# Performance work log

Measured on AMD Instinct MI355X. Metric: run time of the kernel, lower is better.

The kernel has to match this reference:

```python
import jax, jax.numpy as jnp
import numpy as np

DEPTH = 8
IN_FEATURES = 512
OUT_FEATURES = 256
LEAF_COUNT = 2 ** DEPTH          # 256
GATE_COUNT = LEAF_COUNT - 1      # 255
BATCH = 65536


def setup_inputs() -> dict:
    key = jax.random.key(0)
    k1, k2, k3 = jax.random.split(key, 3)
    x = jax.random.normal(k1, (BATCH, IN_FEATURES), dtype=jnp.float32)
    # gw stored transposed as (in_features, gate_count), kaiming-like scale
    gw = jax.random.normal(k2, (IN_FEATURES, GATE_COUNT), dtype=jnp.float32) * (1.0 / np.sqrt(IN_FEATURES))
    gb = jnp.zeros((GATE_COUNT,), dtype=jnp.float32)
    z = jax.random.normal(k3, (OUT_FEATURES, LEAF_COUNT), dtype=jnp.float32)
    return {"x": x, "gw": gw, "gb": gb, "z": z}


def _leaf_probs(x, gw, gb):
    # gatings: (B, gate_count); node it's left child (2p+1) uses g, right child (2p+2) uses 1-g
    g = jax.nn.sigmoid(x @ gw + gb)
    B = x.shape[0]
    dens = jnp.ones((B, 1), dtype=x.dtype)
    for d in range(DEPTH):  # level-wise vectorized traversal, O(depth) steps
        lo, hi = 2 ** d - 1, 2 ** (d + 1) - 1
        gl = g[:, lo:hi]  # (B, 2^d) gatings at this level
        # interleave [parent*g, parent*(1-g)] -> children order matches heap layout
        dens = jnp.stack([dens * gl, dens * (1.0 - gl)], axis=-1).reshape(B, -1)
    return dens  # (B, leaf_count)


def reference(x, gw, gb, z):
    leaf = _leaf_probs(x, gw, gb)        # (B, L)
    # constant projection: z @ leaf_probs^T, then transpose -> (B, out)
    return leaf @ z.T
```

## Files before the change

kernel.cpp:

```cpp
#include <hip/hip_runtime.h>
#include <hip/hip_bf16.h>
#include <stdint.h>


typedef short bf16x8 __attribute__((ext_vector_type(8)));
typedef float f32x4  __attribute__((ext_vector_type(4)));

__device__ __forceinline__ unsigned short f2bf(float f) {
    union { float f; uint32_t u; } c; c.f = f;
    uint32_t u = c.u;
    return (unsigned short)((u + 0x7FFFu + ((u >> 16) & 1u)) >> 16);
}

__device__ __forceinline__ uint32_t pkbf(float a, float b) {
    union { __hip_bfloat162 h; uint32_t u; } cv;
    cv.h = __float22bfloat162_rn(make_float2(a, b));
    return cv.u;
}

__global__ __launch_bounds__(256) void softtree_prep(
    const float* __restrict__ gw, const float* __restrict__ z,
    unsigned short* __restrict__ gwt, unsigned short* __restrict__ zb)
{
    if (blockIdx.x < 32) {
        __shared__ float tsm[64][65];
        const int k0 = (blockIdx.x >> 2) * 64;
        const int n0 = (blockIdx.x & 3) * 64;
        const int r = threadIdx.x >> 6;
        const int c = threadIdx.x & 63;
        const int n = n0 + c;
        #pragma unroll
        for (int i = 0; i < 16; ++i) {
            int kk = r + i * 4;
            tsm[kk][c] = (n < 255) ? gw[(size_t)(k0 + kk) * 255 + n] : 0.0f;
        }
        __syncthreads();
        #pragma unroll
        for (int i = 0; i < 16; ++i) {
            int nn = r + i * 4;
            gwt[(size_t)(n0 + nn) * 512 + k0 + c] = f2bf(tsm[c][nn]);
        }
    } else {
        int base = (blockIdx.x - 32) * 1024 + threadIdx.x * 4;
        const float4 v = *(const float4*)(z + base);
        ushort4 o;
        o.x = f2bf(v.x); o.y = f2bf(v.y); o.z = f2bf(v.z); o.w = f2bf(v.w);
        *(ushort4*)(zb + base) = o;
    }
}

__global__ __launch_bounds__(512, 4) void softtree_main(
    const float* __restrict__ x, const float* __restrict__ gb,
    const unsigned short* __restrict__ gwt, const unsigned short* __restrict__ zb,
    float* __restrict__ out)
{
    __shared__ char smraw[81920];
    float* gs = (float*)smraw;

    const int tid  = threadIdx.x;
    const int lane = tid & 63;
    const int wv   = tid >> 6;
    const int q    = lane >> 4;
    const int l15  = lane & 15;
    const int wr   = wv & 3;
    const int wc   = wv >> 2;
    const int R0   = blockIdx.x * 128;

    const int xrow = tid >> 3;
    const int xkg  = (tid & 7) ^ (xrow & 7);
    const float* xp0 = x + (size_t)(R0 + xrow) * 512 + xkg * 8;
    const float* xp1 = xp0 + (size_t)64 * 512;
    char* xsw0 = smraw + 65536 + tid * 16;
    char* xsw1 = xsw0 + 8192;

    const int ggate_b = wv * 32 + (lane >> 3);
    const int gkg     = (lane & 7) ^ ((lane >> 3) & 7);
    const unsigned short* gwp[4];
    #pragma unroll
    for (int j = 0; j < 4; ++j)
        gwp[j] = gwt + (size_t)(ggate_b + j * 8) * 512 + gkg * 8;
    const uint32_t gwLds = (uint32_t)(wv * 4) * 1024;

    f32x4 acc[2][8];
    #pragma unroll
    for (int t = 0; t < 2; ++t)
        #pragma unroll
        for (int i = 0; i < 8; ++i) acc[t][i] = (f32x4){0.f, 0.f, 0.f, 0.f};

    float4 xa0 = *(const float4*)(xp0);
    float4 xb0 = *(const float4*)(xp0 + 4);
    float4 xa1 = *(const float4*)(xp1);
    float4 xb1 = *(const float4*)(xp1 + 4);
    #pragma unroll
    for (int j = 0; j < 4; ++j)
        __builtin_amdgcn_global_load_lds(
            (const __attribute__((address_space(1))) void*)(gwp[j]),
            (__attribute__((address_space(3))) void*)(smraw + gwLds + j * 1024),
            16, 0, 0);

    for (int kc = 0; kc < 8; ++kc) {
        const int buf = kc & 1;
        __syncthreads();

        union { uint4 u4; uint32_t u[4]; } w0, w1;
        w0.u[0] = pkbf(xa0.x, xa0.y); w0.u[1] = pkbf(xa0.z, xa0.w);
        w0.u[2] = pkbf(xb0.x, xb0.y); w0.u[3] = pkbf(xb0.z, xb0.w);
        w1.u[0] = pkbf(xa1.x, xa1.y); w1.u[1] = pkbf(xa1.z, xa1.w);
        w1.u[2] = pkbf(xb1.x, xb1.y); w1.u[3] = pkbf(xb1.z, xb1.w);
        *(uint4*)xsw0 = w0.u4;
        *(uint4*)xsw1 = w1.u4;

        __syncthreads();

        if (kc < 7) {
            const int ko = (kc + 1) * 64;
            #pragma unroll
            for (int j = 0; j < 4; ++j)
                __builtin_amdgcn_global_load_lds(
                    (const __attribute__((address_space(1))) void*)(gwp[j] + ko),
                    (__attribute__((address_space(3))) void*)(smraw + (buf ^ 1) * 32768 + gwLds + j * 1024),
                    16, 0, 0);
            xa0 = *(const float4*)(xp0 + ko);
            xb0 = *(const float4*)(xp0 + ko + 4);
            xa1 = *(const float4*)(xp1 + ko);
            xb1 = *(const float4*)(xp1 + ko + 4);
        }

        #pragma unroll
        for (int s = 0; s < 2; ++s) {
            const int jx = (4 * s + q) ^ (l15 & 7);
            bf16x8 a0 = *(const bf16x8*)(smraw + 65536 + ((16 * wr + l15) * 8 + jx) * 16);
            bf16x8 a1 = *(const bf16x8*)(smraw + 65536 + 8192 + ((16 * wr + l15) * 8 + jx) * 16);
            #pragma unroll
            for (int nt = 0; nt < 8; ++nt) {
                const int gate = 128 * wc + nt * 16 + l15;
                bf16x8 b = *(const bf16x8*)(smraw + buf * 32768 + (gate * 8 + jx) * 16);
                acc[0][nt] = __builtin_amdgcn_mfma_f32_16x16x32_bf16(a0, b, acc[0][nt], 0, 0, 0);
                acc[1][nt] = __builtin_amdgcn_mfma_f32_16x16x32_bf16(a1, b, acc[1][nt], 0, 0, 0);
            }
        }
    }

    float gbv[8];
    #pragma unroll
    for (int nt = 0; nt < 8; ++nt) {
        int col = 128 * wc + nt * 16 + l15;
        gbv[nt] = (col < 255) ? gb[col] : 0.0f;
    }

    for (int t = 0; t < 2; ++t) {
        __syncthreads();

        #pragma unroll
        for (int nt = 0; nt < 8; ++nt) {
            const int col = 128 * wc + nt * 16 + l15;
            #pragma unroll
            for (int r = 0; r < 4; ++r) {
                const int rowl = 16 * wr + 4 * q + r;
                float v = acc[t][nt][r] + gbv[nt];
                gs[rowl * 258 + col] = 1.0f / (1.0f + __expf(-v));
            }
        }
        __syncthreads();

        const float* gr = gs + (16 * wr + l15) * 258;
        float g0v = gr[0];
        float t1v[2] = { g0v, 1.0f - g0v };
        float t2v[4], t3v[8];
        #pragma unroll
        for (int u = 0; u < 2; ++u) {
            float gl = gr[1 + u];
            t2v[2 * u] = t1v[u] * gl; t2v[2 * u + 1] = t1v[u] - t2v[2 * u];
        }
        #pragma unroll
        for (int u = 0; u < 4; ++u) {
            float gl = gr[3 + u];
            t3v[2 * u] = t2v[u] * gl; t3v[2 * u + 1] = t2v[u] - t3v[2 * u];
        }
        bf16x8 a2[8];
        #pragma unroll
        for (int c = 0; c < 8; ++c) {
            const int G = c * 4 + q;
            float p = t3v[c];
            float g3 = gr[7 + c];
            p = (q & 2) ? (p - p * g3) : (p * g3);
            float g4 = gr[15 + 2 * c + (q >> 1)];
            p = (q & 1) ? (p - p * g4) : (p * g4);
            float g5 = gr[31 + G];
            float a0 = p * g5, a1 = p - a0;
            float g6a = gr[63 + 2 * G], g6b = gr[64 + 2 * G];
            float b00 = a0 * g6a, b01 = a0 - b00;
            float b10 = a1 * g6b, b11 = a1 - b10;
            float g70 = gr[127 + 4 * G], g71 = gr[128 + 4 * G];
            float g72 = gr[129 + 4 * G], g73 = gr[130 + 4 * G];
            float lf0 = b00 * g70, lf1 = b00 - lf0;
            float lf2 = b01 * g71, lf3 = b01 - lf2;
            float lf4 = b10 * g72, lf5 = b10 - lf4;
            float lf6 = b11 * g73, lf7 = b11 - lf6;
            union { bf16x8 v; uint32_t u[4]; } pk;
            pk.u[0] = pkbf(lf0, lf1);
            pk.u[1] = pkbf(lf2, lf3);
            pk.u[2] = pkbf(lf4, lf5);
            pk.u[3] = pkbf(lf6, lf7);
            a2[c] = pk.v;
        }

        f32x4 acc2[8];
        #pragma unroll
        for (int i = 0; i < 8; ++i) acc2[i] = (f32x4){0.f, 0.f, 0.f, 0.f};
        #pragma unroll
        for (int nt = 0; nt < 8; ++nt) {
            const unsigned short* zrow = zb + (size_t)(128 * wc + nt * 16 + l15) * 256 + q * 8;
            #pragma unroll
            for (int c = 0; c < 8; ++c) {
                bf16x8 b = *(const bf16x8*)(zrow + c * 32);
                acc2[nt] = __builtin_amdgcn_mfma_f32_16x16x32_bf16(a2[c], b, acc2[nt], 0, 0, 0);
            }
        }

        #pragma unroll
        for (int nt = 0; nt < 8; ++nt) {
            const int col = 128 * wc + nt * 16 + l15;
            #pragma unroll
            for (int r = 0; r < 4; ++r) {
                const int row = R0 + t * 64 + 16 * wr + 4 * q + r;
                out[(size_t)row * 256 + col] = acc2[nt][r];
            }
        }
    }
}

extern "C" void kernel_launch(void* const* d_in, const int* in_sizes, int n_in,
                              void* d_out, int out_size, void* d_ws, size_t ws_size,
                              hipStream_t stream) {
    const float* x  = (const float*)d_in[0];
    const float* gw = (const float*)d_in[1];
    const float* gb = (const float*)d_in[2];
    const float* z  = (const float*)d_in[3];
    float* outp = (float*)d_out;

    unsigned short* gwt = (unsigned short*)d_ws;
    unsigned short* zbf = gwt + 256 * 512;

    softtree_prep<<<96, 256, 0, stream>>>(gw, z, gwt, zbf);
    softtree_main<<<512, 512, 0, stream>>>(x, gb, gwt, zbf, outp);
}
```

Measured before the change: 281.8 us.

## Load GEMM operands directly from global memory into registers, dropping LDS staging

The gating GEMM no longer stages x and the bf16 gate weights through double-buffered shared memory with barriers. Each lane now loads its MFMA fragments straight from global memory, converting x to bf16 in registers. Shared memory shrinks to the gate tile used by the epilogue. This removes the block-wide syncs and LDS traffic and may raise occupancy, but it gives up reuse of the weight tile across waves and replaces coalesced global loads with strided per-lane loads that depend on cache hits.

After: 330.1 us. 17.1% more time.

```diff
diff --git a/kernel.cpp b/kernel.cpp
--- a/kernel.cpp
+++ b/kernel.cpp
@@ -54,8 +54,7 @@
     const unsigned short* __restrict__ gwt, const unsigned short* __restrict__ zb,
     float* __restrict__ out)
 {
-    __shared__ char smraw[81920];
-    float* gs = (float*)smraw;
+    __shared__ float gs[64 * 258];
 
     const int tid  = threadIdx.x;
     const int lane = tid & 63;
@@ -66,20 +65,8 @@
     const int wc   = wv >> 2;
     const int R0   = blockIdx.x * 128;
 
-    const int xrow = tid >> 3;
-    const int xkg  = (tid & 7) ^ (xrow & 7);
-    const float* xp0 = x + (size_t)(R0 + xrow) * 512 + xkg * 8;
-    const float* xp1 = xp0 + (size_t)64 * 512;
-    char* xsw0 = smraw + 65536 + tid * 16;
-    char* xsw1 = xsw0 + 8192;
-
-    const int ggate_b = wv * 32 + (lane >> 3);
-    const int gkg     = (lane & 7) ^ ((lane >> 3) & 7);
-    const unsigned short* gwp[4];
-    #pragma unroll
-    for (int j = 0; j < 4; ++j)
-        gwp[j] = gwt + (size_t)(ggate_b + j * 8) * 512 + gkg * 8;
-    const uint32_t gwLds = (uint32_t)(wv * 4) * 1024;
+    const float* xr = x + (size_t)(R0 + 16 * wr + l15) * 512 + 8 * q;
+    const unsigned short* bp = gwt + (size_t)(128 * wc + l15) * 512 + 8 * q;
 
     f32x4 acc[2][8];
     #pragma unroll
@@ -87,54 +74,31 @@
         #pragma unroll
         for (int i = 0; i < 8; ++i) acc[t][i] = (f32x4){0.f, 0.f, 0.f, 0.f};
 
-    float4 xa0 = *(const float4*)(xp0);
-    float4 xb0 = *(const float4*)(xp0 + 4);
-    float4 xa1 = *(const float4*)(xp1);
-    float4 xb1 = *(const float4*)(xp1 + 4);
-    #pragma unroll
-    for (int j = 0; j < 4; ++j)
-        __builtin_amdgcn_global_load_lds(
-            (const __attribute__((address_space(1))) void*)(gwp[j]),
-            (__attribute__((address_space(3))) void*)(smraw + gwLds + j * 1024),
-            16, 0, 0);
-
+    #pragma unroll 2
     for (int kc = 0; kc < 8; ++kc) {
-        const int buf = kc & 1;
-        __syncthreads();
-
-        union { uint4 u4; uint32_t u[4]; } w0, w1;
-        w0.u[0] = pkbf(xa0.x, xa0.y); w0.u[1] = pkbf(xa0.z, xa0.w);
-        w0.u[2] = pkbf(xb0.x, xb0.y); w0.u[3] = pkbf(xb0.z, xb0.w);
-        w1.u[0] = pkbf(xa1.x, xa1.y); w1.u[1] = pkbf(xa1.z, xa1.w);
-        w1.u[2] = pkbf(xb1.x, xb1.y); w1.u[3] = pkbf(xb1.z, xb1.w);
-        *(uint4*)xsw0 = w0.u4;
-        *(uint4*)xsw1 = w1.u4;
-
-        __syncthreads();
-
-        if (kc < 7) {
-            const int ko = (kc + 1) * 64;
-            #pragma unroll
-            for (int j = 0; j < 4; ++j)
-                __builtin_amdgcn_global_load_lds(
-                    (const __attribute__((address_space(1))) void*)(gwp[j] + ko),
-                    (__attribute__((address_space(3))) void*)(smraw + (buf ^ 1) * 32768 + gwLds + j * 1024),
-                    16, 0, 0);
-            xa0 = *(const float4*)(xp0 + ko);
-            xb0 = *(const float4*)(xp0 + ko + 4);
-            xa1 = *(const float4*)(xp1 + ko);
-            xb1 = *(const float4*)(xp1 + ko + 4);
-        }
-
         #pragma unroll
         for (int s = 0; s < 2; ++s) {
-            const int jx = (4 * s + q) ^ (l15 & 7);
-            bf16x8 a0 = *(const bf16x8*)(smraw + 65536 + ((16 * wr + l15) * 8 + jx) * 16);
-            bf16x8 a1 = *(const bf16x8*)(smraw + 65536 + 8192 + ((16 * wr + l15) * 8 + jx) * 16);
+            const int ko = kc * 64 + 32 * s;
+            bf16x8 a0, a1;
+            {
+                const float4 v0 = *(const float4*)(xr + ko);
+                const float4 v1 = *(const float4*)(xr + ko + 4);
+                union { bf16x8 v; uint32_t u[4]; } pk;
+                pk.u[0] = pkbf(v0.x, v0.y); pk.u[1] = pkbf(v0.z, v0.w);
+                pk.u[2] = pkbf(v1.x, v1.y); pk.u[3] = pkbf(v1.z, v1.w);
+                a0 = pk.v;
+            }
+            {
+                const float4 v0 = *(const float4*)(xr + 32768 + ko);
+                const float4 v1 = *(const float4*)(xr + 32768 + ko + 4);
+                union { bf16x8 v; uint32_t u[4]; } pk;
+                pk.u[0] = pkbf(v0.x, v0.y); pk.u[1] = pkbf(v0.z, v0.w);
+                pk.u[2] = pkbf(v1.x, v1.y); pk.u[3] = pkbf(v1.z, v1.w);
+                a1 = pk.v;
+            }
             #pragma unroll
             for (int nt = 0; nt < 8; ++nt) {
-                const int gate = 128 * wc + nt * 16 + l15;
-                bf16x8 b = *(const bf16x8*)(smraw + buf * 32768 + (gate * 8 + jx) * 16);
+                const bf16x8 b = *(const bf16x8*)(bp + (size_t)nt * 8192 + ko);
                 acc[0][nt] = __builtin_amdgcn_mfma_f32_16x16x32_bf16(a0, b, acc[0][nt], 0, 0, 0);
                 acc[1][nt] = __builtin_amdgcn_mfma_f32_16x16x32_bf16(a1, b, acc[1][nt], 0, 0, 0);
             }
```
